# Kernel optimization log

Measured on AMD Instinct MI355X. Metric: run time of the kernel, lower is better.

## Reference

```python
import jax, jax.numpy as jnp
import numpy as np

RADIUS = 2  # kernel_size=5 -> r = (5-1)//2
EPS = 1e-8


def _diff(x, r, axis):
    # sliding-window sum from a cumsum along `axis` (same trick as BoxFilter.diff_x/diff_y)
    def sl(a, b):
        idx = [slice(None)] * x.ndim
        idx[axis] = slice(a, b)
        return x[tuple(idx)]
    left = sl(r, 2 * r + 1)
    middle = sl(2 * r + 1, None) - sl(None, -2 * r - 1)
    right = sl(-1, None) - sl(-2 * r - 1, -r - 1)
    return jnp.concatenate([left, middle, right], axis=axis)


def box_filter(x, r):
    # cumsum over H then window-diff, cumsum over W then window-diff
    return _diff(_diff(jnp.cumsum(x, axis=2), r, 2).cumsum(axis=3), r, 3)


def resize_bilinear_align_corners(x, out_h, out_w):
    # x: [N, C, h, w] -> [N, C, out_h, out_w], align_corners=True
    n, c, h, w = x.shape
    ys = jnp.linspace(0.0, h - 1.0, out_h, dtype=x.dtype)
    xs = jnp.linspace(0.0, w - 1.0, out_w, dtype=x.dtype)
    y0 = jnp.floor(ys).astype(jnp.int32)
    x0 = jnp.floor(xs).astype(jnp.int32)
    y1 = jnp.minimum(y0 + 1, h - 1)
    x1 = jnp.minimum(x0 + 1, w - 1)
    wy = (ys - y0.astype(x.dtype))[None, None, :, None]
    wx = (xs - x0.astype(x.dtype))[None, None, None, :]
    rows = x[:, :, y0, :] * (1 - wy) + x[:, :, y1, :] * wy  # [N,C,out_h,w]
    out = rows[:, :, :, x0] * (1 - wx) + rows[:, :, :, x1] * wx
    return out


def setup_inputs() -> dict:
    key = jax.random.key(0)
    k1, k2, k3 = jax.random.split(key, 3)
    return {
        "input_lowres": jax.random.uniform(k1, (8, 3, 256, 256), dtype=jnp.float32),
        "guide_lowres": jax.random.uniform(k2, (8, 3, 256, 256), dtype=jnp.float32),
        "input_highres": jax.random.uniform(k3, (8, 3, 1024, 1024), dtype=jnp.float32),
    }


def reference(input_lowres, guide_lowres, input_highres):
    x_lr, y_lr, x_hr = input_lowres, guide_lowres, input_highres
    r = RADIUS
    _, _, h_lr, w_lr = x_lr.shape
    _, _, h_hr, w_hr = x_hr.shape
    N = box_filter(jnp.ones((1, 1, h_lr, w_lr), dtype=x_lr.dtype), r)  # window pixel counts
    mean_x = box_filter(x_lr, r) / N
    mean_y = box_filter(y_lr, r) / N
    cov_xy = box_filter(x_lr * y_lr, r) / N - mean_x * mean_y
    var_x = box_filter(x_lr * x_lr, r) / N - mean_x * mean_x
    A = cov_xy / (var_x + EPS)
    b = mean_y - A * mean_x
    mean_A = resize_bilinear_align_corners(A, h_hr, w_hr)
    mean_b = resize_bilinear_align_corners(b, h_hr, w_hr)
    return mean_A * x_hr + mean_b
```

## Files before the change

kernel.cpp:

```cpp
#include <hip/hip_runtime.h>


typedef float f4 __attribute__((ext_vector_type(4)));

constexpr int H_LR = 256, W_LR = 256;
constexpr int H_HR = 1024, W_HR = 1024;
constexpr int NC   = 24;
constexpr int RAD  = 2;
constexpr int RPB  = 4;

__global__ void __launch_bounds__(256) fgf_fused(const float* __restrict__ xlr,
                                                 const float* __restrict__ ylr,
                                                 const float* __restrict__ xhr,
                                                 float* __restrict__ out) {
    __shared__ float sx[7][W_LR];
    __shared__ float sy[7][W_LR];
    __shared__ float c0[W_LR], c1[W_LR], c2[W_LR], c3[W_LR];
    __shared__ float sA[3][W_LR], sB[3][W_LR];

    const int c  = blockIdx.y;
    const int i0 = blockIdx.x * RPB;
    const int t  = (int)threadIdx.x;
    const float sc = (float)(H_LR - 1) / (float)(H_HR - 1);

    const size_t hrbase = ((size_t)c << 20) + (size_t)i0 * W_HR + t * 4;
    const f4 xv0 = *(const f4*)(xhr + hrbase);
    const f4 xv1 = *(const f4*)(xhr + hrbase + W_HR);
    const f4 xv2 = *(const f4*)(xhr + hrbase + 2 * W_HR);
    const f4 xv3 = *(const f4*)(xhr + hrbase + 3 * W_HR);

    const int y0min = (int)((float)i0 * sc);

    const int lrbase = c * (H_LR * W_LR);
    for (int idx = t; idx < 7 * 64; idx += 256) {
        const int lr = idx >> 6;
        const int q  = idx & 63;
        const int gr = y0min - 2 + lr;
        f4 vx = {0.f, 0.f, 0.f, 0.f};
        f4 vy = {0.f, 0.f, 0.f, 0.f};
        if (gr >= 0 && gr < H_LR) {
            vx = *(const f4*)(xlr + lrbase + gr * W_LR + q * 4);
            vy = *(const f4*)(ylr + lrbase + gr * W_LR + q * 4);
        }
        *(f4*)&sx[lr][q * 4] = vx;
        *(f4*)&sy[lr][q * 4] = vy;
    }
    __syncthreads();

    for (int rr = 0; rr < 3; ++rr) {
        const int r   = min(y0min + rr, H_LR - 1);
        const int ri0 = max(r - RAD, 0), ri1 = min(r + RAD, H_LR - 1);
        float cx = 0.f, cy = 0.f, cxy = 0.f, cxx = 0.f;
        for (int ii = ri0; ii <= ri1; ++ii) {
            const int l = ii - (y0min - 2);
            const float vx = sx[l][t];
            const float vy = sy[l][t];
            cx += vx; cy += vy; cxy += vx * vy; cxx += vx * vx;
        }
        c0[t] = cx; c1[t] = cy; c2[t] = cxy; c3[t] = cxx;
        __syncthreads();
        const int j0 = max(t - RAD, 0), j1 = min(t + RAD, W_LR - 1);
        float sxs = 0.f, sys = 0.f, sxy = 0.f, sxx = 0.f;
        for (int jj = j0; jj <= j1; ++jj) {
            sxs += c0[jj]; sys += c1[jj]; sxy += c2[jj]; sxx += c3[jj];
        }
        const float inv = 1.0f / (float)((ri1 - ri0 + 1) * (j1 - j0 + 1));
        const float mx  = sxs * inv;
        const float my  = sys * inv;
        const float cov = sxy * inv - mx * my;
        const float var = sxx * inv - mx * mx;
        const float a   = cov / (var + 1e-8f);
        sA[rr][t] = a;
        sB[rr][t] = my - a * mx;
        __syncthreads();
    }

    float ax0[4], ax1[4], ax2[4], bx0[4], bx1[4], bx2[4];
    #pragma unroll
    for (int m = 0; m < 4; ++m) {
        const int   j   = t * 4 + m;
        const float fx  = (float)j * sc;
        const int   x0  = (int)fx;
        const float wx  = fx - (float)x0;
        const int   x1  = min(x0 + 1, W_LR - 1);
        const float wx0 = 1.f - wx;
        ax0[m] = sA[0][x0] * wx0 + sA[0][x1] * wx;
        ax1[m] = sA[1][x0] * wx0 + sA[1][x1] * wx;
        ax2[m] = sA[2][x0] * wx0 + sA[2][x1] * wx;
        bx0[m] = sB[0][x0] * wx0 + sB[0][x1] * wx;
        bx1[m] = sB[1][x0] * wx0 + sB[1][x1] * wx;
        bx2[m] = sB[2][x0] * wx0 + sB[2][x1] * wx;
    }

    #pragma unroll
    for (int k = 0; k < RPB; ++k) {
        const int   i   = i0 + k;
        const float fy  = (float)i * sc;
        const int   yy0 = (int)fy;
        const float wy  = fy - (float)yy0;
        const int   l0  = yy0 - y0min;
        const int   l1  = min(yy0 + 1, H_LR - 1) - y0min;
        const float w0  = (l0 == 0 ? 1.f - wy : 0.f) + (l1 == 0 ? wy : 0.f);
        const float w1  = (l0 == 1 ? 1.f - wy : 0.f) + (l1 == 1 ? wy : 0.f);
        const float w2  = (l1 == 2 ? wy : 0.f);

        const f4 xvk = (k == 0) ? xv0 : (k == 1) ? xv1 : (k == 2) ? xv2 : xv3;
        f4 ov;
        #pragma unroll
        for (int m = 0; m < 4; ++m) {
            const float a = ax0[m] * w0 + ax1[m] * w1 + ax2[m] * w2;
            const float b = bx0[m] * w0 + bx1[m] * w1 + bx2[m] * w2;
            ov[m] = a * xvk[m] + b;
        }
        __builtin_nontemporal_store(ov, (f4*)(out + hrbase + (size_t)k * W_HR));
    }
}

extern "C" void kernel_launch(void* const* d_in, const int* in_sizes, int n_in,
                              void* d_out, int out_size, void* d_ws, size_t ws_size,
                              hipStream_t stream) {
    const float* x_lr = (const float*)d_in[0];
    const float* y_lr = (const float*)d_in[1];
    const float* x_hr = (const float*)d_in[2];
    float* out = (float*)d_out;

    dim3 grid(H_HR / RPB, NC, 1);
    fgf_fused<<<grid, 256, 0, stream>>>(x_lr, y_lr, x_hr, out);
}
```

Before: 51.08 us.

## Process eight high-res rows per block and restructure low-res box filter stage

Measured after the change: 42.62 us. 16.6% less time.

```diff
diff --git a/kernel.cpp b/kernel.cpp
--- a/kernel.cpp
+++ b/kernel.cpp
@@ -7,34 +7,34 @@
 constexpr int H_HR = 1024, W_HR = 1024;
 constexpr int NC   = 24;
 constexpr int RAD  = 2;
-constexpr int RPB  = 4;
+constexpr int RPB  = 8;
+
+constexpr int CS_W    = W_LR + 4;
+constexpr int CS_BYTES = 4 * CS_W * 4 * 4;
+constexpr int AB_OFF  = CS_BYTES;
 
 __global__ void __launch_bounds__(256) fgf_fused(const float* __restrict__ xlr,
                                                  const float* __restrict__ ylr,
                                                  const float* __restrict__ xhr,
                                                  float* __restrict__ out) {
-    __shared__ float sx[7][W_LR];
-    __shared__ float sy[7][W_LR];
-    __shared__ float c0[W_LR], c1[W_LR], c2[W_LR], c3[W_LR];
-    __shared__ float sA[3][W_LR], sB[3][W_LR];
+    __shared__ __align__(16) char lds[CS_BYTES + 2 * 4 * W_LR * 4];
+    auto sx = reinterpret_cast<float(*)[W_LR]>(lds);
+    auto sy = reinterpret_cast<float(*)[W_LR]>(lds + 8 * W_LR * 4);
+    auto cs = reinterpret_cast<float(*)[CS_W][4]>(lds);
+    auto ab = reinterpret_cast<float(*)[W_LR][2]>(lds + AB_OFF);
 
     const int c  = blockIdx.y;
     const int i0 = blockIdx.x * RPB;
     const int t  = (int)threadIdx.x;
-    const float sc = (float)(H_LR - 1) / (float)(H_HR - 1);
+    const float scale = (float)(H_LR - 1) / (float)(H_HR - 1);
 
-    const size_t hrbase = ((size_t)c << 20) + (size_t)i0 * W_HR + t * 4;
-    const f4 xv0 = *(const f4*)(xhr + hrbase);
-    const f4 xv1 = *(const f4*)(xhr + hrbase + W_HR);
-    const f4 xv2 = *(const f4*)(xhr + hrbase + 2 * W_HR);
-    const f4 xv3 = *(const f4*)(xhr + hrbase + 3 * W_HR);
-
-    const int y0min = (int)((float)i0 * sc);
+    const int y0min = (int)((float)i0 * scale);
 
     const int lrbase = c * (H_LR * W_LR);
-    for (int idx = t; idx < 7 * 64; idx += 256) {
-        const int lr = idx >> 6;
-        const int q  = idx & 63;
+    #pragma unroll
+    for (int half = 0; half < 2; ++half) {
+        const int idx = half * 256 + t;
+        const int lr = idx >> 6, q = idx & 63;
         const int gr = y0min - 2 + lr;
         f4 vx = {0.f, 0.f, 0.f, 0.f};
         f4 vy = {0.f, 0.f, 0.f, 0.f};
@@ -47,70 +47,87 @@
     }
     __syncthreads();
 
-    for (int rr = 0; rr < 3; ++rr) {
-        const int r   = min(y0min + rr, H_LR - 1);
-        const int ri0 = max(r - RAD, 0), ri1 = min(r + RAD, H_LR - 1);
-        float cx = 0.f, cy = 0.f, cxy = 0.f, cxx = 0.f;
-        for (int ii = ri0; ii <= ri1; ++ii) {
-            const int l = ii - (y0min - 2);
-            const float vx = sx[l][t];
-            const float vy = sy[l][t];
-            cx += vx; cy += vy; cxy += vx * vy; cxx += vx * vx;
+    float vx[8], vy[8];
+    #pragma unroll
+    for (int l = 0; l < 8; ++l) { vx[l] = sx[l][t]; vy[l] = sy[l][t]; }
+    __syncthreads();
+
+    #pragma unroll
+    for (int rr = 0; rr < 4; ++rr) {
+        float a = 0.f, b = 0.f, cxy = 0.f, cxx = 0.f;
+        #pragma unroll
+        for (int l = rr; l < rr + 5; ++l) {
+            a += vx[l]; b += vy[l]; cxy += vx[l] * vy[l]; cxx += vx[l] * vx[l];
         }
-        c0[t] = cx; c1[t] = cy; c2[t] = cxy; c3[t] = cxx;
-        __syncthreads();
-        const int j0 = max(t - RAD, 0), j1 = min(t + RAD, W_LR - 1);
-        float sxs = 0.f, sys = 0.f, sxy = 0.f, sxx = 0.f;
-        for (int jj = j0; jj <= j1; ++jj) {
-            sxs += c0[jj]; sys += c1[jj]; sxy += c2[jj]; sxx += c3[jj];
+        f4 v = {a, b, cxy, cxx};
+        *(f4*)&cs[rr][t + 2][0] = v;
+    }
+    if (t < 2) {
+        const f4 z = {0.f, 0.f, 0.f, 0.f};
+        #pragma unroll
+        for (int rr = 0; rr < 4; ++rr) {
+            *(f4*)&cs[rr][t][0] = z;
+            *(f4*)&cs[rr][t + W_LR + 2][0] = z;
         }
-        const float inv = 1.0f / (float)((ri1 - ri0 + 1) * (j1 - j0 + 1));
-        const float mx  = sxs * inv;
-        const float my  = sys * inv;
-        const float cov = sxy * inv - mx * my;
-        const float var = sxx * inv - mx * mx;
+    }
+    __syncthreads();
+
+    const int hcnt = min(t + RAD, W_LR - 1) - max(t - RAD, 0) + 1;
+    #pragma unroll
+    for (int rr = 0; rr < 4; ++rr) {
+        f4 s = {0.f, 0.f, 0.f, 0.f};
+        #pragma unroll
+        for (int d = 0; d < 5; ++d) s += *(const f4*)&cs[rr][t + d][0];
+        const int r  = y0min + rr;
+        const int v0 = max(r - RAD, 0), v1 = min(r + RAD, H_LR - 1);
+        const float inv = 1.0f / (float)((v1 - v0 + 1) * hcnt);
+        const float mx  = s.x * inv;
+        const float my  = s.y * inv;
+        const float cov = s.z * inv - mx * my;
+        const float var = s.w * inv - mx * mx;
         const float a   = cov / (var + 1e-8f);
-        sA[rr][t] = a;
-        sB[rr][t] = my - a * mx;
-        __syncthreads();
+        ab[rr][t][0] = a;
+        ab[rr][t][1] = my - a * mx;
     }
+    __syncthreads();
 
-    float ax0[4], ax1[4], ax2[4], bx0[4], bx1[4], bx2[4];
+    float ax[4][4], bx[4][4];
     #pragma unroll
     for (int m = 0; m < 4; ++m) {
         const int   j   = t * 4 + m;
-        const float fx  = (float)j * sc;
+        const float fx  = (float)j * scale;
         const int   x0  = (int)fx;
         const float wx  = fx - (float)x0;
         const int   x1  = min(x0 + 1, W_LR - 1);
         const float wx0 = 1.f - wx;
-        ax0[m] = sA[0][x0] * wx0 + sA[0][x1] * wx;
-        ax1[m] = sA[1][x0] * wx0 + sA[1][x1] * wx;
-        ax2[m] = sA[2][x0] * wx0 + sA[2][x1] * wx;
-        bx0[m] = sB[0][x0] * wx0 + sB[0][x1] * wx;
-        bx1[m] = sB[1][x0] * wx0 + sB[1][x1] * wx;
-        bx2[m] = sB[2][x0] * wx0 + sB[2][x1] * wx;
+        #pragma unroll
+        for (int rr = 0; rr < 4; ++rr) {
+            ax[rr][m] = ab[rr][x0][0] * wx0 + ab[rr][x1][0] * wx;
+            bx[rr][m] = ab[rr][x0][1] * wx0 + ab[rr][x1][1] * wx;
+        }
     }
 
+    const size_t hrbase = ((size_t)c << 20) + (size_t)i0 * W_HR + t * 4;
     #pragma unroll
     for (int k = 0; k < RPB; ++k) {
         const int   i   = i0 + k;
-        const float fy  = (float)i * sc;
+        const float fy  = (float)i * scale;
         const int   yy0 = (int)fy;
         const float wy  = fy - (float)yy0;
         const int   l0  = yy0 - y0min;
         const int   l1  = min(yy0 + 1, H_LR - 1) - y0min;
         const float w0  = (l0 == 0 ? 1.f - wy : 0.f) + (l1 == 0 ? wy : 0.f);
         const float w1  = (l0 == 1 ? 1.f - wy : 0.f) + (l1 == 1 ? wy : 0.f);
-        const float w2  = (l1 == 2 ? wy : 0.f);
+        const float w2  = (l0 == 2 ? 1.f - wy : 0.f) + (l1 == 2 ? wy : 0.f);
+        const float w3  = (l1 == 3 ? wy : 0.f);
 
-        const f4 xvk = (k == 0) ? xv0 : (k == 1) ? xv1 : (k == 2) ? xv2 : xv3;
+        const f4 xv = *(const f4*)(xhr + hrbase + (size_t)k * W_HR);
         f4 ov;
         #pragma unroll
         for (int m = 0; m < 4; ++m) {
-            const float a = ax0[m] * w0 + ax1[m] * w1 + ax2[m] * w2;
-            const float b = bx0[m] * w0 + bx1[m] * w1 + bx2[m] * w2;
-            ov[m] = a * xvk[m] + b;
+            const float a = ax[0][m] * w0 + ax[1][m] * w1 + ax[2][m] * w2 + ax[3][m] * w3;
+            const float b = bx[0][m] * w0 + bx[1][m] * w1 + bx[2][m] * w2 + bx[3][m] * w3;
+            ov[m] = a * xv[m] + b;
         }
         __builtin_nontemporal_store(ov, (f4*)(out + hrbase + (size_t)k * W_HR));
     }
```
